# Kernel optimization log

Hardware: AMD Instinct MI355X
Metric: run time of the kernel (lower is better)

Reference implementation:

```python
import jax, jax.numpy as jnp
import numpy as np

H = 16  # n_heads

def _rmsnorm(x, g, eps=1e-6):
    return x * jax.lax.rsqrt(jnp.mean(x * x, axis=-1, keepdims=True) + eps) * g

def _rope_diag(L, hd, dtype):
    # Diagonal of the full [L, hd, hd] rotary matrix: cos(pos * theta_pair) at every dim.
    # (The torch einsum 'bhld,ldd->bhld' extracts this diagonal, so no pairwise rotation occurs.)
    pair = jnp.arange(hd) // 2
    theta = 10000.0 ** (-2.0 * pair / hd)
    return jnp.cos(jnp.arange(L)[:, None].astype(jnp.float32) * theta[None, :]).astype(dtype)


def setup_inputs() -> dict:
    key = jax.random.key(0)
    ks = jax.random.split(key, 8)
    B, L, E = 2, 2048, 2048
    F = 2 * E  # SwiGLU width
    s = 0.02
    return {
        "x": jax.random.normal(ks[0], (B, L, E), jnp.float32),
        "g": jnp.ones((E,), jnp.float32),
        "wq": jax.random.normal(ks[1], (E, E), jnp.float32) * s,
        "wk": jax.random.normal(ks[2], (E, E), jnp.float32) * s,
        "wv": jax.random.normal(ks[3], (E, E), jnp.float32) * s,
        "w1": jax.random.normal(ks[4], (E, F), jnp.float32) * s,
        "b1": jnp.zeros((F,), jnp.float32),
        "wg": jax.random.normal(ks[5], (F, F), jnp.float32) * s,
        "bg": jnp.zeros((F,), jnp.float32),
        "wl": jax.random.normal(ks[6], (F, F), jnp.float32) * s,
        "bl": jnp.zeros((F,), jnp.float32),
        "beta": jnp.ones((1,), jnp.float32),
        "w2": jax.random.normal(ks[7], (F, E), jnp.float32) * s,
        "b2": jnp.zeros((E,), jnp.float32),
    }


def reference(x, g, wq, wk, wv, w1, b1, wg, bg, wl, bl, beta, w2, b2):
    B, L, E = x.shape
    hd = E // H
    x_res = x
    h = _rmsnorm(x, g)
    # projections -> [B, H, L, hd]
    q = (h @ wq).reshape(B, L, H, hd).transpose(0, 2, 1, 3)
    k = (h @ wk).reshape(B, L, H, hd).transpose(0, 2, 1, 3)
    v = (h @ wv).reshape(B, L, H, hd).transpose(0, 2, 1, 3)
    D = _rope_diag(L, hd, x.dtype)  # [L, hd], diagonal of rotary matrix
    q = q * D
    k = k * D
    score = jnp.einsum('bhld,bhmd->bhlm', q, k)  # [B,H,L,L]
    # causal mask added BEFORE scaling (faithful to source)
    mask = jnp.triu(jnp.full((L, L), -jnp.inf, dtype=score.dtype), k=1)
    score = (score + mask) / jnp.sqrt(jnp.asarray(hd, score.dtype))
    attn = jax.nn.softmax(score, axis=-1)
    o = jnp.einsum('bhlm,bhmd->bhld', attn, v)
    o = o.transpose(0, 2, 1, 3).reshape(B, L, E)
    x = o + x_res
    x_res = x
    h = _rmsnorm(x, g)
    h = h @ w1 + b1  # [B, L, 2E]
    gate = h @ wg + bg
    lin = h @ wl + bl
    act = gate * jax.nn.sigmoid(beta * gate) * lin
    out = act @ w2 + b2
    return out + x_res
```

## Files before the change

### kernel.cpp

```cpp
#include <hip/hip_runtime.h>
#include <cstdint>
#include <math.h>


typedef _Float16 f16;
typedef _Float16 f16x8 __attribute__((ext_vector_type(8)));
typedef _Float16 f16x4 __attribute__((ext_vector_type(4)));
typedef float    f32x4 __attribute__((ext_vector_type(4)));

#define MFMA_16x16x32(a, b, c) __builtin_amdgcn_mfma_f32_16x16x32_f16(a, b, c, 0, 0, 0)

__device__ __forceinline__ void gload_lds16(const void* g, void* lds) {
  __builtin_amdgcn_global_load_lds(
      (__attribute__((address_space(1))) void*)(uintptr_t)g,
      (__attribute__((address_space(3))) void*)(unsigned)(uintptr_t)lds,
      16, 0, 0);
}

__global__ void convT_k(const float* __restrict__ W, f16* __restrict__ Wt,
                        int K, int N) {
  __shared__ float tile[32][33];
  const int n0 = blockIdx.x << 5, k0 = blockIdx.y << 5;
  const int t = threadIdx.x;
  const int r = t >> 3, c4 = (t & 7) << 2;
  const f32x4 v = *(const f32x4*)(W + (size_t)(k0 + r) * N + n0 + c4);
  tile[r][c4 + 0] = v[0]; tile[r][c4 + 1] = v[1];
  tile[r][c4 + 2] = v[2]; tile[r][c4 + 3] = v[3];
  __syncthreads();
  f16x4 o;
  o[0] = (f16)tile[c4 + 0][r]; o[1] = (f16)tile[c4 + 1][r];
  o[2] = (f16)tile[c4 + 2][r]; o[3] = (f16)tile[c4 + 3][r];
  *(f16x4*)(Wt + (size_t)(n0 + r) * K + k0 + c4) = o;
}

__global__ void rope_tab_k(float* __restrict__ Dt) {
  const int l = blockIdx.x, d = threadIdx.x;
  const float th = __expf(-0.0719557841f * (float)(d & ~1));
  Dt[(l << 7) + d] = cosf((float)l * th);
}

__global__ void rmsnorm_k(const float* __restrict__ X, const float* __restrict__ G,
                          f16* __restrict__ H) {
  __shared__ float red[4];
  const int row = blockIdx.x, t = threadIdx.x;
  const float* xp = X + ((size_t)row << 11) + (t << 3);
  const f32x4 v0 = *(const f32x4*)xp;
  const f32x4 v1 = *(const f32x4*)(xp + 4);
  float ss = v0[0]*v0[0] + v0[1]*v0[1] + v0[2]*v0[2] + v0[3]*v0[3]
           + v1[0]*v1[0] + v1[1]*v1[1] + v1[2]*v1[2] + v1[3]*v1[3];
#pragma unroll
  for (int m = 1; m < 64; m <<= 1) ss += __shfl_xor(ss, m);
  if ((t & 63) == 0) red[t >> 6] = ss;
  __syncthreads();
  const float tot = red[0] + red[1] + red[2] + red[3];
  const float rs = rsqrtf(tot * (1.f / 2048.f) + 1e-6f);
  const float* gp = G + (t << 3);
  const f32x4 g0 = *(const f32x4*)gp, g1 = *(const f32x4*)(gp + 4);
  f16x8 o;
  o[0] = (f16)(v0[0]*rs*g0[0]); o[1] = (f16)(v0[1]*rs*g0[1]);
  o[2] = (f16)(v0[2]*rs*g0[2]); o[3] = (f16)(v0[3]*rs*g0[3]);
  o[4] = (f16)(v1[0]*rs*g1[0]); o[5] = (f16)(v1[1]*rs*g1[1]);
  o[6] = (f16)(v1[2]*rs*g1[2]); o[7] = (f16)(v1[3]*rs*g1[3]);
  *(f16x8*)(H + ((size_t)row << 11) + (t << 3)) = o;
}

__global__ void rmsnorm_h_k(const f16* __restrict__ X, const float* __restrict__ G,
                            f16* __restrict__ H) {
  __shared__ float red[4];
  const int row = blockIdx.x, t = threadIdx.x;
  const f16x8 v = *(const f16x8*)(X + ((size_t)row << 11) + (t << 3));
  float f[8];
#pragma unroll
  for (int i = 0; i < 8; ++i) f[i] = (float)v[i];
  float ss = 0.f;
#pragma unroll
  for (int i = 0; i < 8; ++i) ss += f[i] * f[i];
#pragma unroll
  for (int m = 1; m < 64; m <<= 1) ss += __shfl_xor(ss, m);
  if ((t & 63) == 0) red[t >> 6] = ss;
  __syncthreads();
  const float tot = red[0] + red[1] + red[2] + red[3];
  const float rs = rsqrtf(tot * (1.f / 2048.f) + 1e-6f);
  const float* gp = G + (t << 3);
  const f32x4 g0 = *(const f32x4*)gp, g1 = *(const f32x4*)(gp + 4);
  f16x8 o;
#pragma unroll
  for (int i = 0; i < 4; ++i) o[i] = (f16)(f[i] * rs * g0[i]);
#pragma unroll
  for (int i = 0; i < 4; ++i) o[4 + i] = (f16)(f[4 + i] * rs * g1[i]);
  *(f16x8*)(H + ((size_t)row << 11) + (t << 3)) = o;
}

__global__ void vtrans_k(const f16* __restrict__ V, f16* __restrict__ Vt) {
  __shared__ f16 tile[32][36];
  const int l0 = blockIdx.x << 5, d0 = blockIdx.y << 5, bh = blockIdx.z;
  const int b = bh >> 4, h = bh & 15;
  const int t = threadIdx.x;
  const int r = t >> 3, c4 = (t & 7) << 2;
  const f16x4 v = *(const f16x4*)(V + (size_t)((b << 11) + l0 + r) * 2048 + (h << 7) + d0 + c4);
  tile[r][c4 + 0] = v[0]; tile[r][c4 + 1] = v[1];
  tile[r][c4 + 2] = v[2]; tile[r][c4 + 3] = v[3];
  __syncthreads();
  f16x4 o;
  o[0] = tile[c4 + 0][r]; o[1] = tile[c4 + 1][r];
  o[2] = tile[c4 + 2][r]; o[3] = tile[c4 + 3][r];
  *(f16x4*)(Vt + (size_t)((bh << 7) + d0 + r) * 2048 + l0 + c4) = o;
}

template <int EPI>
__launch_bounds__(512, 2)
__global__ void gemm256_k(const f16* __restrict__ A, const f16* __restrict__ Bt,
                          void* __restrict__ Cout, int M, int N, int K,
                          const float* __restrict__ bias,
                          const f16* __restrict__ auxh,
                          const float* __restrict__ betap) {
  __shared__ alignas(16) f16 lds[65536];
  const int t = threadIdx.x, lane = t & 63, w = t >> 6;
  const int wm = w >> 2, wn = w & 3;
  const int bm = blockIdx.y << 8, bn = blockIdx.x << 8;
  const int lh = lane & 15, lq = lane >> 4;
  const int NT = K >> 6;
  const int lrow = lane >> 3;
  const int lco  = ((lane & 7) ^ lrow) << 3;

  const f16* Agl = A  + (size_t)(bm + lrow) * K + lco;
  const f16* Bgl = Bt + (size_t)(bn + lrow) * K + lco;
  const int aw = w << 3;
  const int bw = w << 4;

  f32x4 acc[8][4] = {};
  f16x8 bf[4][2];

  auto stA = [&](int tile, int half) {
    const int d = (tile & 1) << 15;
    const int k0 = tile << 6;
    const int r0 = aw + (half << 6);
    gload_lds16(Agl + (size_t)r0 * K + k0, (void*)&lds[d + r0 * 64]);
    gload_lds16(Agl + (size_t)(r0 + 128) * K + k0, (void*)&lds[d + (r0 + 128) * 64]);
  };
  auto stB = [&](int tile, int half) {
    const int d = ((tile & 1) << 15) + 16384;
    const int k0 = tile << 6;
    const int r0 = bw + (half << 7);
    gload_lds16(Bgl + (size_t)r0 * K + k0, (void*)&lds[d + r0 * 64]);
    gload_lds16(Bgl + (size_t)(r0 + 8) * K + k0, (void*)&lds[d + (r0 + 8) * 64]);
  };
  auto ldA = [&](int d, int mi, int kk) {
    const int r = (wm << 7) + (mi << 4) + lh;
    return *(const f16x8*)&lds[(d << 15) + r * 64 + ((((kk << 2) + lq) ^ (lh & 7)) << 3)];
  };
  auto ldB = [&](int d, int ni, int kk) {
    const int r = (wn << 6) + (ni << 4) + lh;
    return *(const f16x8*)&lds[(d << 15) + 16384 + r * 64 + ((((kk << 2) + lq) ^ (lh & 7)) << 3)];
  };

  stB(0, 0); stB(0, 1); stA(0, 0); stA(0, 1);
  stB(1, 0); stB(1, 1); stA(1, 0);
  asm volatile("s_waitcnt vmcnt(6)" ::: "memory");
  __builtin_amdgcn_s_barrier();

  for (int tt = 0; tt < NT; tt += 2) {
    const bool pf = (tt + 2 < NT);
#pragma unroll
    for (int hf = 0; hf < 2; ++hf) {
#pragma unroll
      for (int ph = 0; ph < 4; ++ph) {
        f16x8 a0k0 = ldA(hf, 2 * ph, 0),     a0k1 = ldA(hf, 2 * ph, 1);
        f16x8 a1k0 = ldA(hf, 2 * ph + 1, 0), a1k1 = ldA(hf, 2 * ph + 1, 1);
        if (ph == 0) {
#pragma unroll
          for (int ni = 0; ni < 4; ++ni) {
            bf[ni][0] = ldB(hf, ni, 0); bf[ni][1] = ldB(hf, ni, 1);
          }
        }
        if (hf == 0) {
          if (ph == 0) stA(tt + 1, 1);
          else if (ph == 1) { if (pf) stB(tt + 2, 0); }
          else if (ph == 2) { if (pf) stB(tt + 2, 1); }
          else              { if (pf) stA(tt + 2, 0); }
        } else {
          if (ph == 0)      { if (pf) stA(tt + 2, 1); }
          else if (ph == 1) { if (pf) stB(tt + 3, 0); }
          else if (ph == 2) { if (pf) stB(tt + 3, 1); }
          else              { if (pf) stA(tt + 3, 0); }
        }
        __builtin_amdgcn_s_barrier();
        __builtin_amdgcn_s_setprio(1);
#pragma unroll
        for (int ni = 0; ni < 4; ++ni) {
          acc[2 * ph][ni]     = MFMA_16x16x32(a0k0, bf[ni][0], acc[2 * ph][ni]);
          acc[2 * ph][ni]     = MFMA_16x16x32(a0k1, bf[ni][1], acc[2 * ph][ni]);
          acc[2 * ph + 1][ni] = MFMA_16x16x32(a1k0, bf[ni][0], acc[2 * ph + 1][ni]);
          acc[2 * ph + 1][ni] = MFMA_16x16x32(a1k1, bf[ni][1], acc[2 * ph + 1][ni]);
        }
        __builtin_amdgcn_s_setprio(0);
        if (ph == 3) {
          if (hf == 0) {
            if (pf) asm volatile("s_waitcnt vmcnt(6)" ::: "memory");
            else    asm volatile("s_waitcnt vmcnt(0)" ::: "memory");
          } else if (pf) {
            asm volatile("s_waitcnt vmcnt(6)" ::: "memory");
          }
        }
        __builtin_amdgcn_s_barrier();
      }
    }
  }

  const float be = (EPI == 3) ? betap[0] : 0.f;
#pragma unroll
  for (int mi = 0; mi < 8; ++mi) {
#pragma unroll
    for (int ni = 0; ni < 4; ++ni) {
#pragma unroll
      for (int r = 0; r < 4; ++r) {
        const int grow = bm + (wm << 7) + (mi << 4) + (lq << 2) + r;
        const int gcol = bn + (wn << 6) + (ni << 4) + lh;
        float v = acc[mi][ni][r] + bias[gcol];
        const size_t off = (size_t)grow * N + gcol;
        if (EPI == 2) {
          ((f16*)Cout)[off] = (f16)v;
        } else if (EPI == 3) {
          ((f16*)Cout)[off] = (f16)(v / (1.f + __expf(-be * v)));
        } else {
          ((f16*)Cout)[off] = (f16)(v * (float)auxh[off]);
        }
      }
    }
  }
}

template <int EPI>
__launch_bounds__(256, 3)
__global__ void gemm_k(const f16* __restrict__ A, const f16* __restrict__ Bt,
                       void* __restrict__ Cout, int M, int N, int K,
                       const float* __restrict__ bias,
                       const float* __restrict__ auxf,
                       const f16* __restrict__ auxh,
                       float scale) {
  __shared__ alignas(16) f16 As[128 * 64];
  __shared__ alignas(16) f16 Bs[128 * 64];
  const int t = threadIdx.x;
  const int lane = t & 63;
  const int w = t >> 6;
  const int wm = w >> 1, wn = w & 1;
  const int bm = blockIdx.y << 7;
  const int bn = blockIdx.x << 7;
  const int lh = lane & 15, lq = lane >> 4;

  f32x4 acc[4][4] = {};

  for (int k0 = 0; k0 < K; k0 += 64) {
    __syncthreads();
#pragma unroll
    for (int i = 0; i < 4; ++i) {
      const int idx = i * 256 + (w << 6) + lane;
      const int row = idx >> 3, c = idx & 7;
      const int cs = (c ^ (row & 7)) << 3;
      gload_lds16(A + (size_t)(bm + row) * K + k0 + cs,
                  &As[(i * 256 + (w << 6)) << 3]);
      gload_lds16(Bt + (size_t)(bn + row) * K + k0 + cs,
                  &Bs[(i * 256 + (w << 6)) << 3]);
    }
    asm volatile("s_waitcnt vmcnt(0)" ::: "memory");
    __syncthreads();
#pragma unroll
    for (int kk = 0; kk < 2; ++kk) {
      f16x8 af[4], bfr[4];
#pragma unroll
      for (int mi = 0; mi < 4; ++mi) {
        const int r = (wm << 6) + (mi << 4) + lh;
        af[mi] = *(const f16x8*)&As[(r << 6) + ((((kk << 2) + lq) ^ (r & 7)) << 3)];
      }
#pragma unroll
      for (int ni = 0; ni < 4; ++ni) {
        const int r = (wn << 6) + (ni << 4) + lh;
        bfr[ni] = *(const f16x8*)&Bs[(r << 6) + ((((kk << 2) + lq) ^ (r & 7)) << 3)];
      }
#pragma unroll
      for (int mi = 0; mi < 4; ++mi)
#pragma unroll
        for (int ni = 0; ni < 4; ++ni)
          acc[mi][ni] = MFMA_16x16x32(af[mi], bfr[ni], acc[mi][ni]);
    }
  }

#pragma unroll
  for (int mi = 0; mi < 4; ++mi) {
#pragma unroll
    for (int ni = 0; ni < 4; ++ni) {
#pragma unroll
      for (int r = 0; r < 4; ++r) {
        const int grow = bm + (wm << 6) + (mi << 4) + (lq << 2) + r;
        const int gcol = bn + (wn << 6) + (ni << 4) + lh;
        float v = acc[mi][ni][r];
        if (EPI == 6) {
          const int seg = gcol >> 11, c = gcol & 2047;
          if (seg < 2) {
            const float f = auxf[((grow & 2047) << 7) + (c & 127)];
            v *= (seg == 0) ? scale * f : f;
          }
          ((f16*)Cout)[(size_t)seg * 8388608 + ((size_t)grow << 11) + c] = (f16)v;
        } else if (EPI == 1) {
          ((f16*)Cout)[(size_t)grow * N + gcol] = (f16)v;
        } else {
          ((float*)Cout)[(size_t)grow * N + gcol] = v + bias[gcol] + (float)auxh[(size_t)grow * N + gcol];
        }
      }
    }
  }
}

__launch_bounds__(256, 2)
__global__ void attn_k(const f16* __restrict__ Q, const f16* __restrict__ Kb,
                       const f16* __restrict__ Vt, const float* __restrict__ Xres,
                       f16* __restrict__ X2, int* __restrict__ qcnt) {
  constexpr int L = 2048, E = 2048, HD = 128;
  __shared__ alignas(16) f16 Ks[2][64 * 128];
  __shared__ alignas(16) f16 Vs[128 * 64];
  __shared__ alignas(16) f16 Ps[4][32 * 72];
  __shared__ int s_item;

  const int t = threadIdx.x, lane = t & 63, w = t >> 6;
  const int lh = lane & 15, lq = lane >> 4;

  for (;;) {
    if (t == 0) s_item = atomicAdd(qcnt, 1);
    __syncthreads();
    const int item = s_item;
    if (item >= 512) return;
    const int bh = item & 31;
    const int q0 = (15 - (item >> 5)) << 7;
    const int b = bh >> 4, h = bh & 15;
    const int wrow0 = q0 + (w << 5);

    auto issueK = [&](int kv0, int buf) {
#pragma unroll
      for (int i = 0; i < 4; ++i) {
        const int idx = i * 256 + (w << 6) + lane;
        const int row = idx >> 4, c = idx & 15;
        gload_lds16(Kb + (size_t)(b * L + kv0 + row) * E + h * HD + ((c ^ (row & 7)) << 3),
                    &Ks[buf][(i * 256 + (w << 6)) << 3]);
      }
    };
    auto issueV = [&](int kv0) {
#pragma unroll
      for (int i = 0; i < 4; ++i) {
        const int idx = i * 256 + (w << 6) + lane;
        const int row = idx >> 3, c = idx & 7;
        gload_lds16(Vt + ((size_t)bh * HD + row) * L + kv0 + ((c ^ (row & 7)) << 3),
                    &Vs[(i * 256 + (w << 6)) << 3]);
      }
    };

    f16x8 qf[2][4];
#pragma unroll
    for (int mi = 0; mi < 2; ++mi) {
      const f16* qrow = Q + (size_t)(b * L + wrow0 + (mi << 4) + lh) * E + h * HD;
#pragma unroll
      for (int kq = 0; kq < 4; ++kq)
        qf[mi][kq] = *(const f16x8*)(qrow + (kq << 5) + (lq << 3));
    }
    asm volatile("s_waitcnt vmcnt(0)" ::: "memory");

    f32x4 oacc[2][8] = {};
    float mrun[2][4], lrun[2][4];
#pragma unroll
    for (int mi = 0; mi < 2; ++mi)
#pragma unroll
      for (int r = 0; r < 4; ++r) { mrun[mi][r] = -1e30f; lrun[mi][r] = 0.f; }

    const int nt = (q0 + 128) >> 6;
    issueK(0, 0);
    for (int it = 0; it < nt; ++it) {
      const int cur = it & 1;
      const int kv0 = it << 6;
      const bool more = (it + 1 < nt);
      issueV(kv0);
      if (more) {
        issueK(kv0 + 64, cur ^ 1);
        asm volatile("s_waitcnt vmcnt(8)" ::: "memory");
      } else {
        asm volatile("s_waitcnt vmcnt(4)" ::: "memory");
      }
      __builtin_amdgcn_s_barrier();

      const bool active = (kv0 <= wrow0 + 31);
      if (active) {
        f32x4 sacc[2][4] = {};
#pragma unroll
        for (int kq = 0; kq < 4; ++kq) {
          f16x8 kf[4];
#pragma unroll
          for (int ni = 0; ni < 4; ++ni) {
            const int r = (ni << 4) + lh;
            kf[ni] = *(const f16x8*)&Ks[cur][(r << 7) + ((((kq << 2) + lq) ^ (r & 7)) << 3)];
          }
#pragma unroll
          for (int mi = 0; mi < 2; ++mi)
#pragma unroll
            for (int ni = 0; ni < 4; ++ni)
              sacc[mi][ni] = MFMA_16x16x32(qf[mi][kq], kf[ni], sacc[mi][ni]);
        }
        if (kv0 + 63 > wrow0) {
#pragma unroll
          for (int mi = 0; mi < 2; ++mi)
#pragma unroll
            for (int ni = 0; ni < 4; ++ni)
#pragma unroll
              for (int r = 0; r < 4; ++r) {
                const int qr = wrow0 + (mi << 4) + (lq << 2) + r;
                const int kv = kv0 + (ni << 4) + lh;
                if (kv > qr) sacc[mi][ni][r] = -1e30f;
              }
        }
        float scl[2][4], rsum[2][4];
#pragma unroll
        for (int mi = 0; mi < 2; ++mi)
#pragma unroll
          for (int r = 0; r < 4; ++r) {
            float v = fmaxf(fmaxf(sacc[mi][0][r], sacc[mi][1][r]),
                            fmaxf(sacc[mi][2][r], sacc[mi][3][r]));
            v = fmaxf(v, __shfl_xor(v, 1));
            v = fmaxf(v, __shfl_xor(v, 2));
            v = fmaxf(v, __shfl_xor(v, 4));
            v = fmaxf(v, __shfl_xor(v, 8));
            const float mnew = fmaxf(mrun[mi][r], v);
            scl[mi][r] = __expf(mrun[mi][r] - mnew);
            mrun[mi][r] = mnew;
            rsum[mi][r] = 0.f;
          }
#pragma unroll
        for (int mi = 0; mi < 2; ++mi)
#pragma unroll
          for (int ni = 0; ni < 4; ++ni)
#pragma unroll
            for (int r = 0; r < 4; ++r) {
              const float p = __expf(sacc[mi][ni][r] - mrun[mi][r]);
              rsum[mi][r] += p;
              Ps[w][((mi << 4) + (lq << 2) + r) * 72 + (ni << 4) + lh] = (f16)p;
            }
#pragma unroll
        for (int mi = 0; mi < 2; ++mi)
#pragma unroll
          for (int r = 0; r < 4; ++r) {
            float s = rsum[mi][r];
            s += __shfl_xor(s, 1);
            s += __shfl_xor(s, 2);
            s += __shfl_xor(s, 4);
            s += __shfl_xor(s, 8);
            lrun[mi][r] = lrun[mi][r] * scl[mi][r] + s;
          }
#pragma unroll
        for (int mi = 0; mi < 2; ++mi)
#pragma unroll
          for (int nd = 0; nd < 8; ++nd)
#pragma unroll
            for (int r = 0; r < 4; ++r) oacc[mi][nd][r] *= scl[mi][r];
      }

      if (more) asm volatile("s_waitcnt vmcnt(4)" ::: "memory");
      else      asm volatile("s_waitcnt vmcnt(0)" ::: "memory");
      __builtin_amdgcn_s_barrier();

      if (active) {
#pragma unroll
        for (int kp = 0; kp < 2; ++kp) {
          f16x8 pf[2];
#pragma unroll
          for (int mi = 0; mi < 2; ++mi)
            pf[mi] = *(const f16x8*)&Ps[w][((mi << 4) + lh) * 72 + (kp << 5) + (lq << 3)];
#pragma unroll
          for (int nd = 0; nd < 8; ++nd) {
            const int r = (nd << 4) + lh;
            const f16x8 vf = *(const f16x8*)&Vs[(r << 6) + ((((kp << 2) + lq) ^ (r & 7)) << 3)];
#pragma unroll
            for (int mi = 0; mi < 2; ++mi)
              oacc[mi][nd] = MFMA_16x16x32(pf[mi], vf, oacc[mi][nd]);
          }
        }
      }
      asm volatile("" ::: "memory");
      __builtin_amdgcn_s_barrier();
    }
#pragma unroll
    for (int mi = 0; mi < 2; ++mi)
#pragma unroll
      for (int nd = 0; nd < 8; ++nd)
#pragma unroll
        for (int r = 0; r < 4; ++r) {
          const int qr = wrow0 + (mi << 4) + (lq << 2) + r;
          const size_t off = (size_t)(b * L + qr) * E + h * HD + (nd << 4) + lh;
          X2[off] = (f16)(oacc[mi][nd][r] / lrun[mi][r] + Xres[off]);
        }
  }
}

extern "C" void kernel_launch(void* const* d_in, const int* in_sizes, int n_in,
                              void* d_out, int out_size, void* d_ws, size_t ws_size,
                              hipStream_t stream) {
  const float* x    = (const float*)d_in[0];
  const float* g    = (const float*)d_in[1];
  const float* wq   = (const float*)d_in[2];
  const float* wk   = (const float*)d_in[3];
  const float* wv   = (const float*)d_in[4];
  const float* w1   = (const float*)d_in[5];
  const float* b1   = (const float*)d_in[6];
  const float* wgp  = (const float*)d_in[7];
  const float* bg   = (const float*)d_in[8];
  const float* wl   = (const float*)d_in[9];
  const float* bl   = (const float*)d_in[10];
  const float* beta = (const float*)d_in[11];
  const float* w2   = (const float*)d_in[12];
  const float* b2   = (const float*)d_in[13];

  constexpr size_t MB = 1ull << 20;
  char* ws = (char*)d_ws;
  f16*   wT   = (f16*)(ws + 0 * MB);
  int*   qcnt = (int*)(ws + 31 * MB);
  float* Dt   = (float*)(ws + 32 * MB);
  f16*   hbuf = (f16*)(ws + 33 * MB);
  f16*   qkv  = (f16*)(ws + 49 * MB);
  f16*   vbuf = (f16*)(ws + 81 * MB);
  f16*   vtb  = (f16*)(ws + 97 * MB);
  f16*   x2h  = (f16*)(ws + 113 * MB);
  f16*   a1   = (f16*)(ws + 49 * MB);
  f16*   sbuf = (f16*)(ws + 81 * MB);
  f16*   act  = (f16*)(ws + 145 * MB);
  (void)ws_size; (void)n_in; (void)in_sizes; (void)out_size;

  const dim3 blk(256);
  const float qscale = 0.08838834764831845f;

  rope_tab_k<<<2048, 128, 0, stream>>>(Dt);
  rmsnorm_k<<<4096, blk, 0, stream>>>(x, g, hbuf);
  hipMemsetAsync(qcnt, 0, 4, stream);

  convT_k<<<dim3(64, 64), blk, 0, stream>>>(wq, wT, 2048, 2048);
  convT_k<<<dim3(64, 64), blk, 0, stream>>>(wk, wT + (size_t)2048 * 2048, 2048, 2048);
  convT_k<<<dim3(64, 64), blk, 0, stream>>>(wv, wT + (size_t)4096 * 2048, 2048, 2048);
  gemm_k<6><<<dim3(48, 32), blk, 0, stream>>>(hbuf, wT, qkv, 4096, 6144, 2048,
                                              nullptr, Dt, nullptr, qscale);
  vtrans_k<<<dim3(64, 4, 32), blk, 0, stream>>>(vbuf, vtb);

  attn_k<<<384, blk, 0, stream>>>(qkv, qkv + (size_t)8388608, vtb, x, x2h, qcnt);

  rmsnorm_h_k<<<4096, blk, 0, stream>>>(x2h, g, hbuf);

  convT_k<<<dim3(128, 64), blk, 0, stream>>>(w1, wT, 2048, 4096);
  gemm256_k<2><<<dim3(16, 16), 512, 0, stream>>>(hbuf, wT, a1, 4096, 4096, 2048,
                                                 b1, nullptr, nullptr);
  convT_k<<<dim3(128, 128), blk, 0, stream>>>(wgp, wT, 4096, 4096);
  gemm256_k<3><<<dim3(16, 16), 512, 0, stream>>>(a1, wT, sbuf, 4096, 4096, 4096,
                                                 bg, nullptr, beta);
  convT_k<<<dim3(128, 128), blk, 0, stream>>>(wl, wT, 4096, 4096);
  gemm256_k<4><<<dim3(16, 16), 512, 0, stream>>>(a1, wT, act, 4096, 4096, 4096,
                                                 bl, sbuf, nullptr);
  convT_k<<<dim3(64, 128), blk, 0, stream>>>(w2, wT, 4096, 2048);
  gemm_k<5><<<dim3(16, 32), blk, 0, stream>>>(act, wT, (float*)d_out, 4096, 2048, 4096,
                                              b2, nullptr, x2h, 1.0f);
}
```

Measured before the change: 723.5 us.

## Fuse gate and linear SwiGLU GEMMs into one interleaved-weight GEMM

Packs the gate and linear weights into one interleaved transposed matrix, with 128-column blocks alternating, so a single 256-wide tile GEMM computes both gate and lin for the same 128 output columns. The epilogue stages lin through LDS and applies swish(gate)*lin in-register, writing act directly. This removes the intermediate sbuf write and re-read and a separate kernel launch, while re-reading a1 once instead of twice. In exchange, half the waves sit idle during the final multiply and an extra block barrier plus LDS round-trip is added to the epilogue.

```diff
diff --git a/kernel.cpp b/kernel.cpp
--- a/kernel.cpp
+++ b/kernel.cpp
@@ -33,6 +33,24 @@
   *(f16x4*)(Wt + (size_t)(n0 + r) * K + k0 + c4) = o;
 }
 
+__global__ void convT_pack_k(const float* __restrict__ W, f16* __restrict__ Wt,
+                             int K, int N, int off) {
+  __shared__ float tile[32][33];
+  const int n0 = blockIdx.x << 5, k0 = blockIdx.y << 5;
+  const int t = threadIdx.x;
+  const int r = t >> 3, c4 = (t & 7) << 2;
+  const f32x4 v = *(const f32x4*)(W + (size_t)(k0 + r) * N + n0 + c4);
+  tile[r][c4 + 0] = v[0]; tile[r][c4 + 1] = v[1];
+  tile[r][c4 + 2] = v[2]; tile[r][c4 + 3] = v[3];
+  __syncthreads();
+  f16x4 o;
+  o[0] = (f16)tile[c4 + 0][r]; o[1] = (f16)tile[c4 + 1][r];
+  o[2] = (f16)tile[c4 + 2][r]; o[3] = (f16)tile[c4 + 3][r];
+  const int n = n0 + r;
+  const int pr = ((n >> 7) << 8) + off + (n & 127);
+  *(f16x4*)(Wt + (size_t)pr * K + k0 + c4) = o;
+}
+
 __global__ void rope_tab_k(float* __restrict__ Dt) {
   const int l = blockIdx.x, d = threadIdx.x;
   const float th = __expf(-0.0719557841f * (float)(d & ~1));
@@ -112,7 +130,7 @@
 __global__ void gemm256_k(const f16* __restrict__ A, const f16* __restrict__ Bt,
                           void* __restrict__ Cout, int M, int N, int K,
                           const float* __restrict__ bias,
-                          const f16* __restrict__ auxh,
+                          const float* __restrict__ bias2,
                           const float* __restrict__ betap) {
   __shared__ alignas(16) f16 lds[65536];
   const int t = threadIdx.x, lane = t & 63, w = t >> 6;
@@ -207,25 +225,51 @@
     }
   }
 
-  const float be = (EPI == 3) ? betap[0] : 0.f;
-#pragma unroll
-  for (int mi = 0; mi < 8; ++mi) {
-#pragma unroll
-    for (int ni = 0; ni < 4; ++ni) {
-#pragma unroll
-      for (int r = 0; r < 4; ++r) {
-        const int grow = bm + (wm << 7) + (mi << 4) + (lq << 2) + r;
-        const int gcol = bn + (wn << 6) + (ni << 4) + lh;
-        float v = acc[mi][ni][r] + bias[gcol];
-        const size_t off = (size_t)grow * N + gcol;
-        if (EPI == 2) {
-          ((f16*)Cout)[off] = (f16)v;
-        } else if (EPI == 3) {
-          ((f16*)Cout)[off] = (f16)(v / (1.f + __expf(-be * v)));
-        } else {
-          ((f16*)Cout)[off] = (f16)(v * (float)auxh[off]);
-        }
-      }
+  if (EPI == 2) {
+#pragma unroll
+    for (int mi = 0; mi < 8; ++mi) {
+#pragma unroll
+      for (int ni = 0; ni < 4; ++ni) {
+#pragma unroll
+        for (int r = 0; r < 4; ++r) {
+          const int grow = bm + (wm << 7) + (mi << 4) + (lq << 2) + r;
+          const int gcol = bn + (wn << 6) + (ni << 4) + lh;
+          ((f16*)Cout)[(size_t)grow * N + gcol] = (f16)(acc[mi][ni][r] + bias[gcol]);
+        }
+      }
+    }
+  } else {
+    f16* linlds = (f16*)lds;
+    const int ncol0 = bn >> 1;
+    const int Nout = N >> 1;
+    if (wn >= 2) {
+#pragma unroll
+      for (int mi = 0; mi < 8; ++mi)
+#pragma unroll
+        for (int ni = 0; ni < 4; ++ni)
+#pragma unroll
+          for (int r = 0; r < 4; ++r) {
+            const int row = (wm << 7) + (mi << 4) + (lq << 2) + r;
+            const int col = ((wn - 2) << 6) + (ni << 4) + lh;
+            linlds[row * 136 + col] = (f16)(acc[mi][ni][r] + bias2[ncol0 + col]);
+          }
+    }
+    __syncthreads();
+    if (wn < 2) {
+      const float be = betap[0];
+#pragma unroll
+      for (int mi = 0; mi < 8; ++mi)
+#pragma unroll
+        for (int ni = 0; ni < 4; ++ni)
+#pragma unroll
+          for (int r = 0; r < 4; ++r) {
+            const int row = (wm << 7) + (mi << 4) + (lq << 2) + r;
+            const int col = (wn << 6) + (ni << 4) + lh;
+            const float v = acc[mi][ni][r] + bias[ncol0 + col];
+            const float lin = (float)linlds[row * 136 + col];
+            const float a = v / (1.f + __expf(-be * v)) * lin;
+            ((f16*)Cout)[(size_t)(bm + row) * Nout + ncol0 + col] = (f16)a;
+          }
     }
   }
 }
@@ -301,8 +345,6 @@
             v *= (seg == 0) ? scale * f : f;
           }
           ((f16*)Cout)[(size_t)seg * 8388608 + ((size_t)grow << 11) + c] = (f16)v;
-        } else if (EPI == 1) {
-          ((f16*)Cout)[(size_t)grow * N + gcol] = (f16)v;
         } else {
           ((float*)Cout)[(size_t)grow * N + gcol] = v + bias[gcol] + (float)auxh[(size_t)grow * N + gcol];
         }
@@ -516,17 +558,16 @@
 
   constexpr size_t MB = 1ull << 20;
   char* ws = (char*)d_ws;
-  f16*   wT   = (f16*)(ws + 0 * MB);
-  int*   qcnt = (int*)(ws + 31 * MB);
-  float* Dt   = (float*)(ws + 32 * MB);
-  f16*   hbuf = (f16*)(ws + 33 * MB);
-  f16*   qkv  = (f16*)(ws + 49 * MB);
-  f16*   vbuf = (f16*)(ws + 81 * MB);
-  f16*   vtb  = (f16*)(ws + 97 * MB);
-  f16*   x2h  = (f16*)(ws + 113 * MB);
-  f16*   a1   = (f16*)(ws + 49 * MB);
-  f16*   sbuf = (f16*)(ws + 81 * MB);
-  f16*   act  = (f16*)(ws + 145 * MB);
+  f16*   wBIG = (f16*)(ws + 0 * MB);
+  float* Dt   = (float*)(ws + 64 * MB);
+  int*   qcnt = (int*)(ws + 65 * MB);
+  f16*   hbuf = (f16*)(ws + 66 * MB);
+  f16*   qkv  = (f16*)(ws + 82 * MB);
+  f16*   vbuf = (f16*)(ws + 114 * MB);
+  f16*   vtb  = (f16*)(ws + 130 * MB);
+  f16*   x2h  = (f16*)(ws + 146 * MB);
+  f16*   a1   = (f16*)(ws + 82 * MB);
+  f16*   act  = (f16*)(ws + 114 * MB);
   (void)ws_size; (void)n_in; (void)in_sizes; (void)out_size;
 
   const dim3 blk(256);
@@ -536,10 +577,10 @@
   rmsnorm_k<<<4096, blk, 0, stream>>>(x, g, hbuf);
   hipMemsetAsync(qcnt, 0, 4, stream);
 
-  convT_k<<<dim3(64, 64), blk, 0, stream>>>(wq, wT, 2048, 2048);
-  convT_k<<<dim3(64, 64), blk, 0, stream>>>(wk, wT + (size_t)2048 * 2048, 2048, 2048);
-  convT_k<<<dim3(64, 64), blk, 0, stream>>>(wv, wT + (size_t)4096 * 2048, 2048, 2048);
-  gemm_k<6><<<dim3(48, 32), blk, 0, stream>>>(hbuf, wT, qkv, 4096, 6144, 2048,
+  convT_k<<<dim3(64, 64), blk, 0, stream>>>(wq, wBIG, 2048, 2048);
+  convT_k<<<dim3(64, 64), blk, 0, stream>>>(wk, wBIG + (size_t)2048 * 2048, 2048, 2048);
+  convT_k<<<dim3(64, 64), blk, 0, stream>>>(wv, wBIG + (size_t)4096 * 2048, 2048, 2048);
+  gemm_k<6><<<dim3(48, 32), blk, 0, stream>>>(hbuf, wBIG, qkv, 4096, 6144, 2048,
                                               nullptr, Dt, nullptr, qscale);
   vtrans_k<<<dim3(64, 4, 32), blk, 0, stream>>>(vbuf, vtb);
 
@@ -547,16 +588,14 @@
 
   rmsnorm_h_k<<<4096, blk, 0, stream>>>(x2h, g, hbuf);
 
-  convT_k<<<dim3(128, 64), blk, 0, stream>>>(w1, wT, 2048, 4096);
-  gemm256_k<2><<<dim3(16, 16), 512, 0, stream>>>(hbuf, wT, a1, 4096, 4096, 2048,
+  convT_k<<<dim3(128, 64), blk, 0, stream>>>(w1, wBIG, 2048, 4096);
+  gemm256_k<2><<<dim3(16, 16), 512, 0, stream>>>(hbuf, wBIG, a1, 4096, 4096, 2048,
                                                  b1, nullptr, nullptr);
-  convT_k<<<dim3(128, 128), blk, 0, stream>>>(wgp, wT, 4096, 4096);
-  gemm256_k<3><<<dim3(16, 16), 512, 0, stream>>>(a1, wT, sbuf, 4096, 4096, 4096,
-                                                 bg, nullptr, beta);
-  convT_k<<<dim3(128, 128), blk, 0, stream>>>(wl, wT, 4096, 4096);
-  gemm256_k<4><<<dim3(16, 16), 512, 0, stream>>>(a1, wT, act, 4096, 4096, 4096,
-                                                 bl, sbuf, nullptr);
-  convT_k<<<dim3(64, 128), blk, 0, stream>>>(w2, wT, 4096, 2048);
-  gemm_k<5><<<dim3(16, 32), blk, 0, stream>>>(act, wT, (float*)d_out, 4096, 2048, 4096,
+  convT_pack_k<<<dim3(128, 128), blk, 0, stream>>>(wgp, wBIG, 4096, 4096, 0);
+  convT_pack_k<<<dim3(128, 128), blk, 0, stream>>>(wl, wBIG, 4096, 4096, 128);
+  gemm256_k<7><<<dim3(32, 16), 512, 0, stream>>>(a1, wBIG, act, 4096, 8192, 4096,
+                                                 bg, bl, beta);
+  convT_k<<<dim3(64, 128), blk, 0, stream>>>(w2, wBIG, 4096, 2048);
+  gemm_k<5><<<dim3(16, 32), blk, 0, stream>>>(act, wBIG, (float*)d_out, 4096, 2048, 4096,
                                               b2, nullptr, x2h, 1.0f);
 }
```

Measured after the change: 718.2 us. Within noise of the previous version (-0.7%).
